# Kernel optimization log

Hardware: AMD Instinct MI355X
Metric: run time of the kernel (lower is better)

The kernel has to match this reference:

```python
import jax, jax.numpy as jnp
import numpy as np

N, M, D = 1024, 1024, 256


def setup_inputs() -> dict:
    key = jax.random.key(0)
    k1, k2 = jax.random.split(key)
    z_x = jax.random.normal(k1, (N, D), dtype=jnp.float32)
    z_y = jax.random.normal(k2, (M, D), dtype=jnp.float32)
    return {"z_x": z_x, "z_y": z_y}


def reference(z_x, z_y):
    # s[i, j] = -sum_d |z_x[i, d] - z_y[j, d]|   -> [N, M] negative L1 distances
    s = -jnp.sum(jnp.abs(z_x[:, None, :] - z_y[None, :, :]), axis=-1)
    a = jax.nn.softmax(s, axis=1)  # row-wise alignment probs
    b = jax.nn.softmax(s, axis=0)  # column-wise alignment probs
    w = a + b - a * b              # soft symmetric alignment weights
    # weighted mean similarity (scalar)
    c = jnp.sum(w * s) / jnp.sum(w)
    return c
```

## Files before the change

kernel.cpp:

```cpp
#include <hip/hip_runtime.h>
#include <math.h>
#include <string.h>

#define NN 1024
#define MM 1024
#define DD 256
#define TILE 64
#define NTB 16
#define PITCH_H 264

typedef _Float16 f16x2 __attribute__((ext_vector_type(2)));
typedef _Float16 f16x4 __attribute__((ext_vector_type(4)));

__device__ inline f16x2 habs2(f16x2 v) {
  unsigned u = __builtin_bit_cast(unsigned, v) & 0x7FFF7FFFu;
  return __builtin_bit_cast(f16x2, u);
}

__device__ inline float dot2acc(f16x2 a, float acc) {
#if __has_builtin(__builtin_amdgcn_fdot2)
  const f16x2 one = {(_Float16)1.0f, (_Float16)1.0f};
  return __builtin_amdgcn_fdot2(a, one, acc, false);
#else
  return acc + (float)a.x + (float)a.y;
#endif
}

__device__ inline void merge_ms(float& m, float& s, float m2, float s2) {
  float mn = fmaxf(m, m2);
  s = s * __expf(m - mn) + s2 * __expf(m2 - mn);
  m = mn;
}

__device__ inline float wredSum(float v) {
#pragma unroll
  for (int o = 32; o > 0; o >>= 1) v += __shfl_down(v, o, 64);
  return v;
}

__global__ __launch_bounds__(256) void k_tile(const float* __restrict__ zx,
                                              const float* __restrict__ zy,
                                              float* __restrict__ S,
                                              float* __restrict__ rowPM,
                                              float* __restrict__ rowPS,
                                              float* __restrict__ colPM,
                                              float* __restrict__ colPS,
                                              int* __restrict__ counter) {
  __shared__ __align__(16) _Float16 xs[TILE * PITCH_H];
  __shared__ __align__(16) _Float16 ys[TILE * PITCH_H];
  __shared__ float lm[16][64];
  __shared__ float lsv[16][64];

  const int it = blockIdx.y, jt = blockIdx.x;
  const int i0 = it * TILE, j0 = jt * TILE;
  const int t = threadIdx.x;
  const int tx = t & 15, ty = t >> 4;

  if (it == 0 && jt == 0 && t == 0) counter[0] = 0;

#pragma unroll
  for (int k = 0; k < 16; ++k) {
    int idx4 = t + k * 256;
    int r = idx4 >> 6;
    int c4 = idx4 & 63;
    float4 vx = reinterpret_cast<const float4*>(zx + (size_t)(i0 + r) * DD)[c4];
    float4 vy = reinterpret_cast<const float4*>(zy + (size_t)(j0 + r) * DD)[c4];
    f16x4 hx = {(_Float16)vx.x, (_Float16)vx.y, (_Float16)vx.z, (_Float16)vx.w};
    f16x4 hy = {(_Float16)vy.x, (_Float16)vy.y, (_Float16)vy.z, (_Float16)vy.w};
    *reinterpret_cast<f16x4*>(&xs[r * PITCH_H + c4 * 4]) = hx;
    *reinterpret_cast<f16x4*>(&ys[r * PITCH_H + c4 * 4]) = hy;
  }
  __syncthreads();

  float acc4[4][4] = {{0.f}};
  for (int s8 = 0; s8 < 32; ++s8) {
    uint4 xw[4], yw[4];
#pragma unroll
    for (int a = 0; a < 4; ++a)
      xw[a] = *reinterpret_cast<const uint4*>(&xs[(ty + a * 16) * PITCH_H + s8 * 8]);
#pragma unroll
    for (int b = 0; b < 4; ++b)
      yw[b] = *reinterpret_cast<const uint4*>(&ys[(tx + b * 16) * PITCH_H + s8 * 8]);
#pragma unroll
    for (int a = 0; a < 4; ++a)
#pragma unroll
      for (int b = 0; b < 4; ++b) {
        float acc = acc4[a][b];
        acc = dot2acc(habs2(__builtin_bit_cast(f16x2, xw[a].x) - __builtin_bit_cast(f16x2, yw[b].x)), acc);
        acc = dot2acc(habs2(__builtin_bit_cast(f16x2, xw[a].y) - __builtin_bit_cast(f16x2, yw[b].y)), acc);
        acc = dot2acc(habs2(__builtin_bit_cast(f16x2, xw[a].z) - __builtin_bit_cast(f16x2, yw[b].z)), acc);
        acc = dot2acc(habs2(__builtin_bit_cast(f16x2, xw[a].w) - __builtin_bit_cast(f16x2, yw[b].w)), acc);
        acc4[a][b] = acc;
      }
  }

#pragma unroll
  for (int a = 0; a < 4; ++a) {
    int i = i0 + ty + a * 16;
#pragma unroll
    for (int b = 0; b < 4; ++b) {
      int j = j0 + tx + b * 16;
      S[(size_t)i * MM + j] = -acc4[a][b];
    }
  }

#pragma unroll
  for (int a = 0; a < 4; ++a) {
    float m = -acc4[a][0];
#pragma unroll
    for (int b = 1; b < 4; ++b) m = fmaxf(m, -acc4[a][b]);
    float s = 0.f;
#pragma unroll
    for (int b = 0; b < 4; ++b) s += __expf(-acc4[a][b] - m);
#pragma unroll
    for (int off = 1; off < 16; off <<= 1) {
      float m2 = __shfl_xor(m, off, 64);
      float s2 = __shfl_xor(s, off, 64);
      merge_ms(m, s, m2, s2);
    }
    if (tx == 0) {
      int i = i0 + ty + a * 16;
      rowPM[(size_t)jt * NN + i] = m;
      rowPS[(size_t)jt * NN + i] = s;
    }
  }

#pragma unroll
  for (int b = 0; b < 4; ++b) {
    int c = tx + b * 16;
    float m = -acc4[0][b];
#pragma unroll
    for (int a = 1; a < 4; ++a) m = fmaxf(m, -acc4[a][b]);
    float s = 0.f;
#pragma unroll
    for (int a = 0; a < 4; ++a) s += __expf(-acc4[a][b] - m);
    lm[ty][c] = m;
    lsv[ty][c] = s;
  }
  __syncthreads();
  if (t < 64) {
    float m = lm[0][t], s = lsv[0][t];
#pragma unroll
    for (int k = 1; k < 16; ++k) merge_ms(m, s, lm[k][t], lsv[k][t]);
    colPM[(size_t)it * MM + j0 + t] = m;
    colPS[(size_t)it * MM + j0 + t] = s;
  }
}

__global__ __launch_bounds__(256) void k_wacc(const float* __restrict__ S,
                                              const float* __restrict__ rowPM,
                                              const float* __restrict__ rowPS,
                                              const float* __restrict__ colPM,
                                              const float* __restrict__ colPS,
                                              float* __restrict__ bNum,
                                              float* __restrict__ bDen,
                                              int* __restrict__ counter,
                                              float* __restrict__ out) {
  const int bid = blockIdx.x;
  const int t = threadIdx.x;

  float4 cm = reinterpret_cast<const float4*>(colPM)[t];
  float4 cs = reinterpret_cast<const float4*>(colPS)[t];
#pragma unroll
  for (int k = 1; k < NTB; ++k) {
    float4 m2 = reinterpret_cast<const float4*>(colPM + (size_t)k * MM)[t];
    float4 s2 = reinterpret_cast<const float4*>(colPS + (size_t)k * MM)[t];
    merge_ms(cm.x, cs.x, m2.x, s2.x);
    merge_ms(cm.y, cs.y, m2.y, s2.y);
    merge_ms(cm.z, cs.z, m2.z, s2.z);
    merge_ms(cm.w, cs.w, m2.w, s2.w);
  }
  float4 ci;
  ci.x = 1.f / cs.x; ci.y = 1.f / cs.y; ci.z = 1.f / cs.z; ci.w = 1.f / cs.w;

  __shared__ float rowMl[4], rowIl[4];
  if (t < 4) {
    int r = bid * 4 + t;
    float m = rowPM[r], s = rowPS[r];
#pragma unroll
    for (int k = 1; k < NTB; ++k)
      merge_ms(m, s, rowPM[(size_t)k * NN + r], rowPS[(size_t)k * NN + r]);
    rowMl[t] = m;
    rowIl[t] = 1.f / s;
  }
  __syncthreads();

  float num = 0.f, den = 0.f;
#pragma unroll
  for (int rl = 0; rl < 4; ++rl) {
    int row = bid * 4 + rl;
    float4 v = reinterpret_cast<const float4*>(S + (size_t)row * MM)[t];
    float rm = rowMl[rl], ri = rowIl[rl];
#define DO_COMP(VX, CMX, CIX)                 \
    {                                         \
      float a = __expf((VX) - rm) * ri;       \
      float b = __expf((VX) - (CMX)) * (CIX); \
      float w = a + b - a * b;                \
      num += w * (VX);                        \
      den += w;                               \
    }
    DO_COMP(v.x, cm.x, ci.x)
    DO_COMP(v.y, cm.y, ci.y)
    DO_COMP(v.z, cm.z, ci.z)
    DO_COMP(v.w, cm.w, ci.w)
#undef DO_COMP
  }

  num = wredSum(num);
  den = wredSum(den);
  __shared__ float rn[4], rd[4];
  const int lane = t & 63, wv = t >> 6;
  if (lane == 0) { rn[wv] = num; rd[wv] = den; }
  __syncthreads();
  if (t == 0) {
    bNum[bid] = rn[0] + rn[1] + rn[2] + rn[3];
    bDen[bid] = rd[0] + rd[1] + rd[2] + rd[3];
  }

  __shared__ int isLast;
  if (t == 0) {
    __threadfence();
    int ticket = atomicAdd(counter, 1);
    isLast = (ticket == 255) ? 1 : 0;
  }
  __syncthreads();
  if (isLast) {
    __threadfence();
    float n = bNum[t];
    float d = bDen[t];
    n = wredSum(n);
    d = wredSum(d);
    if (lane == 0) { rn[wv] = n; rd[wv] = d; }
    __syncthreads();
    if (t == 0) out[0] = (rn[0] + rn[1] + rn[2] + rn[3]) / (rd[0] + rd[1] + rd[2] + rd[3]);
  }
}

extern "C" void kernel_launch(void* const* d_in, const int* in_sizes, int n_in,
                              void* d_out, int out_size, void* d_ws, size_t ws_size,
                              hipStream_t stream) {
  const float* zx = (const float*)d_in[0];
  const float* zy = (const float*)d_in[1];
  float* out = (float*)d_out;

  float* ws = (float*)d_ws;
  float* S     = ws;
  float* rowPM = S + (size_t)NN * MM;
  float* rowPS = rowPM + NTB * NN;
  float* colPM = rowPS + NTB * NN;
  float* colPS = colPM + NTB * MM;
  float* bNum  = colPS + NTB * MM;
  float* bDen  = bNum + 256;
  int*   counter = (int*)(bDen + 256);

  k_tile<<<dim3(NTB, NTB), 256, 0, stream>>>(zx, zy, S, rowPM, rowPS, colPM, colPS, counter);
  k_wacc<<<256, 256, 0, stream>>>(S, rowPM, rowPS, colPM, colPS, bNum, bDen, counter, out);
}
```

Measured before the change: 39.35 us.

## Halve row tile to 32 for 512 blocks and split final reduction into separate kernel

The tile kernel now uses 32x64 tiles, so the grid grows from 256 to 512 blocks to fill more of the GPU's compute units, and each thread keeps 2x4 accumulators instead of 4x4. The column partial merge in the second kernel now walks 32 partials instead of 16. The atomic last-block-done pattern is replaced by a third single-block kernel that does the final sum. This trades more redundant zy tile loads and an extra launch for better occupancy and no atomic or fence.

Measured after the change: 37.88 us. 1.04x faster.

```diff
diff --git a/kernel.cpp b/kernel.cpp
--- a/kernel.cpp
+++ b/kernel.cpp
@@ -1,12 +1,13 @@
 #include <hip/hip_runtime.h>
 #include <math.h>
-#include <string.h>
 
 #define NN 1024
 #define MM 1024
 #define DD 256
-#define TILE 64
-#define NTB 16
+#define TI 32
+#define TJ 64
+#define NTI 32
+#define NTJ 16
 #define PITCH_H 264
 
 typedef _Float16 f16x2 __attribute__((ext_vector_type(2)));
@@ -44,45 +45,48 @@
                                               float* __restrict__ rowPM,
                                               float* __restrict__ rowPS,
                                               float* __restrict__ colPM,
-                                              float* __restrict__ colPS,
-                                              int* __restrict__ counter) {
-  __shared__ __align__(16) _Float16 xs[TILE * PITCH_H];
-  __shared__ __align__(16) _Float16 ys[TILE * PITCH_H];
+                                              float* __restrict__ colPS) {
+  __shared__ __align__(16) _Float16 xs[TI * PITCH_H];
+  __shared__ __align__(16) _Float16 ys[TJ * PITCH_H];
   __shared__ float lm[16][64];
   __shared__ float lsv[16][64];
 
   const int it = blockIdx.y, jt = blockIdx.x;
-  const int i0 = it * TILE, j0 = jt * TILE;
+  const int i0 = it * TI, j0 = jt * TJ;
   const int t = threadIdx.x;
   const int tx = t & 15, ty = t >> 4;
 
-  if (it == 0 && jt == 0 && t == 0) counter[0] = 0;
-
+#pragma unroll
+  for (int k = 0; k < 8; ++k) {
+    int idx4 = t + k * 256;
+    int r = idx4 >> 6;
+    int c4 = idx4 & 63;
+    float4 v = reinterpret_cast<const float4*>(zx + (size_t)(i0 + r) * DD)[c4];
+    f16x4 h = {(_Float16)v.x, (_Float16)v.y, (_Float16)v.z, (_Float16)v.w};
+    *reinterpret_cast<f16x4*>(&xs[r * PITCH_H + c4 * 4]) = h;
+  }
 #pragma unroll
   for (int k = 0; k < 16; ++k) {
     int idx4 = t + k * 256;
     int r = idx4 >> 6;
     int c4 = idx4 & 63;
-    float4 vx = reinterpret_cast<const float4*>(zx + (size_t)(i0 + r) * DD)[c4];
-    float4 vy = reinterpret_cast<const float4*>(zy + (size_t)(j0 + r) * DD)[c4];
-    f16x4 hx = {(_Float16)vx.x, (_Float16)vx.y, (_Float16)vx.z, (_Float16)vx.w};
-    f16x4 hy = {(_Float16)vy.x, (_Float16)vy.y, (_Float16)vy.z, (_Float16)vy.w};
-    *reinterpret_cast<f16x4*>(&xs[r * PITCH_H + c4 * 4]) = hx;
-    *reinterpret_cast<f16x4*>(&ys[r * PITCH_H + c4 * 4]) = hy;
-  }
-  __syncthreads();
-
-  float acc4[4][4] = {{0.f}};
+    float4 v = reinterpret_cast<const float4*>(zy + (size_t)(j0 + r) * DD)[c4];
+    f16x4 h = {(_Float16)v.x, (_Float16)v.y, (_Float16)v.z, (_Float16)v.w};
+    *reinterpret_cast<f16x4*>(&ys[r * PITCH_H + c4 * 4]) = h;
+  }
+  __syncthreads();
+
+  float acc4[2][4] = {{0.f}};
   for (int s8 = 0; s8 < 32; ++s8) {
-    uint4 xw[4], yw[4];
-#pragma unroll
-    for (int a = 0; a < 4; ++a)
+    uint4 xw[2], yw[4];
+#pragma unroll
+    for (int a = 0; a < 2; ++a)
       xw[a] = *reinterpret_cast<const uint4*>(&xs[(ty + a * 16) * PITCH_H + s8 * 8]);
 #pragma unroll
     for (int b = 0; b < 4; ++b)
       yw[b] = *reinterpret_cast<const uint4*>(&ys[(tx + b * 16) * PITCH_H + s8 * 8]);
 #pragma unroll
-    for (int a = 0; a < 4; ++a)
+    for (int a = 0; a < 2; ++a)
 #pragma unroll
       for (int b = 0; b < 4; ++b) {
         float acc = acc4[a][b];
@@ -95,7 +99,7 @@
   }
 
 #pragma unroll
-  for (int a = 0; a < 4; ++a) {
+  for (int a = 0; a < 2; ++a) {
     int i = i0 + ty + a * 16;
 #pragma unroll
     for (int b = 0; b < 4; ++b) {
@@ -105,7 +109,7 @@
   }
 
 #pragma unroll
-  for (int a = 0; a < 4; ++a) {
+  for (int a = 0; a < 2; ++a) {
     float m = -acc4[a][0];
 #pragma unroll
     for (int b = 1; b < 4; ++b) m = fmaxf(m, -acc4[a][b]);
@@ -128,12 +132,8 @@
 #pragma unroll
   for (int b = 0; b < 4; ++b) {
     int c = tx + b * 16;
-    float m = -acc4[0][b];
-#pragma unroll
-    for (int a = 1; a < 4; ++a) m = fmaxf(m, -acc4[a][b]);
-    float s = 0.f;
-#pragma unroll
-    for (int a = 0; a < 4; ++a) s += __expf(-acc4[a][b] - m);
+    float m = fmaxf(-acc4[0][b], -acc4[1][b]);
+    float s = __expf(-acc4[0][b] - m) + __expf(-acc4[1][b] - m);
     lm[ty][c] = m;
     lsv[ty][c] = s;
   }
@@ -147,22 +147,20 @@
   }
 }
 
-__global__ __launch_bounds__(256) void k_wacc(const float* __restrict__ S,
+__global__ __launch_bounds__(256) void k_macc(const float* __restrict__ S,
                                               const float* __restrict__ rowPM,
                                               const float* __restrict__ rowPS,
                                               const float* __restrict__ colPM,
                                               const float* __restrict__ colPS,
                                               float* __restrict__ bNum,
-                                              float* __restrict__ bDen,
-                                              int* __restrict__ counter,
-                                              float* __restrict__ out) {
+                                              float* __restrict__ bDen) {
   const int bid = blockIdx.x;
   const int t = threadIdx.x;
 
   float4 cm = reinterpret_cast<const float4*>(colPM)[t];
   float4 cs = reinterpret_cast<const float4*>(colPS)[t];
 #pragma unroll
-  for (int k = 1; k < NTB; ++k) {
+  for (int k = 1; k < NTI; ++k) {
     float4 m2 = reinterpret_cast<const float4*>(colPM + (size_t)k * MM)[t];
     float4 s2 = reinterpret_cast<const float4*>(colPS + (size_t)k * MM)[t];
     merge_ms(cm.x, cs.x, m2.x, s2.x);
@@ -178,7 +176,7 @@
     int r = bid * 4 + t;
     float m = rowPM[r], s = rowPS[r];
 #pragma unroll
-    for (int k = 1; k < NTB; ++k)
+    for (int k = 1; k < NTJ; ++k)
       merge_ms(m, s, rowPM[(size_t)k * NN + r], rowPS[(size_t)k * NN + r]);
     rowMl[t] = m;
     rowIl[t] = 1.f / s;
@@ -216,24 +214,21 @@
     bNum[bid] = rn[0] + rn[1] + rn[2] + rn[3];
     bDen[bid] = rd[0] + rd[1] + rd[2] + rd[3];
   }
-
-  __shared__ int isLast;
-  if (t == 0) {
-    __threadfence();
-    int ticket = atomicAdd(counter, 1);
-    isLast = (ticket == 255) ? 1 : 0;
-  }
-  __syncthreads();
-  if (isLast) {
-    __threadfence();
-    float n = bNum[t];
-    float d = bDen[t];
-    n = wredSum(n);
-    d = wredSum(d);
-    if (lane == 0) { rn[wv] = n; rd[wv] = d; }
-    __syncthreads();
-    if (t == 0) out[0] = (rn[0] + rn[1] + rn[2] + rn[3]) / (rd[0] + rd[1] + rd[2] + rd[3]);
-  }
+}
+
+__global__ __launch_bounds__(256) void k_final(const float* __restrict__ bNum,
+                                               const float* __restrict__ bDen,
+                                               float* __restrict__ out) {
+  const int t = threadIdx.x;
+  float n = bNum[t];
+  float d = bDen[t];
+  n = wredSum(n);
+  d = wredSum(d);
+  __shared__ float rn[4], rd[4];
+  const int lane = t & 63, wv = t >> 6;
+  if (lane == 0) { rn[wv] = n; rd[wv] = d; }
+  __syncthreads();
+  if (t == 0) out[0] = (rn[0] + rn[1] + rn[2] + rn[3]) / (rd[0] + rd[1] + rd[2] + rd[3]);
 }
 
 extern "C" void kernel_launch(void* const* d_in, const int* in_sizes, int n_in,
@@ -246,13 +241,13 @@
   float* ws = (float*)d_ws;
   float* S     = ws;
   float* rowPM = S + (size_t)NN * MM;
-  float* rowPS = rowPM + NTB * NN;
-  float* colPM = rowPS + NTB * NN;
-  float* colPS = colPM + NTB * MM;
-  float* bNum  = colPS + NTB * MM;
+  float* rowPS = rowPM + NTJ * NN;
+  float* colPM = rowPS + NTJ * NN;
+  float* colPS = colPM + NTI * MM;
+  float* bNum  = colPS + NTI * MM;
   float* bDen  = bNum + 256;
-  int*   counter = (int*)(bDen + 256);
-
-  k_tile<<<dim3(NTB, NTB), 256, 0, stream>>>(zx, zy, S, rowPM, rowPS, colPM, colPS, counter);
-  k_wacc<<<256, 256, 0, stream>>>(S, rowPM, rowPS, colPM, colPS, bNum, bDen, counter, out);
-}
+
+  k_tile<<<dim3(NTJ, NTI), 256, 0, stream>>>(zx, zy, S, rowPM, rowPS, colPM, colPS);
+  k_macc<<<256, 256, 0, stream>>>(S, rowPM, rowPS, colPM, colPS, bNum, bDen);
+  k_final<<<1, 256, 0, stream>>>(bNum, bDen, out);
+}
```
